# Optimization experiments

Measured on AMD Instinct MI355X. Metric: run time of the kernel, lower is better.

Reference implementation:

```python
import jax, jax.numpy as jnp
import numpy as np

N = 100000      # nodes
E = 1600000     # edges
F_IN = 256      # nfeat
F_OUT = 128     # out channels


def setup_inputs() -> dict:
    key = jax.random.key(0)
    k1, k2, k3 = jax.random.split(key, 3)
    feature = jax.random.normal(k1, (N, F_IN), dtype=jnp.float32)
    edge_index = jax.random.randint(k2, (2, E), 0, N, dtype=jnp.int32)
    # glorot-ish init for the GCN linear weight
    W = jax.random.normal(k3, (F_IN, F_OUT), dtype=jnp.float32) * (1.0 / np.sqrt(F_IN))
    b = jnp.zeros((F_OUT,), dtype=jnp.float32)
    return {"feature": feature, "edge_index": edge_index, "W": W, "b": b}


def reference(feature, edge_index, W, b):
    # GCNConv (PyG defaults): add self-loops, symmetric normalization,
    # linear transform then scatter-add aggregation to destination nodes.
    x = feature @ W                                   # [N, F_OUT]
    loops = jnp.arange(N, dtype=edge_index.dtype)
    row = jnp.concatenate([edge_index[0], loops])     # source nodes [E+N]
    col = jnp.concatenate([edge_index[1], loops])     # dest   nodes [E+N]
    ones = jnp.ones(row.shape[0], dtype=x.dtype)
    deg = jax.ops.segment_sum(ones, col, num_segments=N)   # in-degree incl. self-loop
    dinv = jnp.where(deg > 0, jax.lax.rsqrt(deg), 0.0)     # deg^{-1/2}
    norm = dinv[row] * dinv[col]                            # [E+N]
    msg = x[row] * norm[:, None]                            # gather + scale
    agg = jax.ops.segment_sum(msg, col, num_segments=N)     # scatter-add
    x_out = jax.nn.relu(agg + b)                            # [N, F_OUT]
    h = jax.nn.sigmoid(jnp.mean(x_out, axis=0))             # [F_OUT]
    return (x_out, h)
```

## Files before the change

kernel.cpp:

```cpp
#include <hip/hip_runtime.h>
#include <hip/hip_bf16.h>

typedef __attribute__((ext_vector_type(8))) short short8;
typedef __attribute__((ext_vector_type(4))) float floatx4;
typedef unsigned short u16;
typedef unsigned int u32;

#define F_IN  256
#define F_OUT 128
#define CAP   64
#define CA    24
#define CB    40
#define NWIN  8
#define PRE   24

__device__ __forceinline__ float bf_lo(u32 u) { return __uint_as_float(u << 16); }
__device__ __forceinline__ float bf_hi(u32 u) { return __uint_as_float(u & 0xffff0000u); }
__device__ __forceinline__ u16 f2bf(float f) {
    u32 u = __float_as_uint(f);
    u += 0x7fffu + ((u >> 16) & 1u);
    return (u16)(u >> 16);
}

__global__ void k_pack(const float* __restrict__ W, u16* __restrict__ Wp,
                       u16* __restrict__ xw, int* __restrict__ zero0,
                       int nzero, int N) {
    int gid = blockIdx.x * 256 + threadIdx.x;
    if (gid < 32768) {
        int f = gid >> 3, j = gid & 7;
        int lane = f & 63, tt = (f >> 6) & 7, kb = f >> 9;
        int m = lane & 15, q = lane >> 4;
        Wp[(size_t)f * 8 + j] = f2bf(W[(kb * 32 + q * 8 + j) * F_OUT + tt * 16 + m]);
    } else if (gid < 32896) {
        int e = gid - 32768;
        int w = e >> 4, m = e & 15;
        xw[((size_t)w * (N + 1) + N) * 16 + m] = 0;
    } else {
        int z = gid - 32896;
        if (z < nzero) zero0[z] = 0;
    }
}

__global__ void k_fillcap_xcd(const int* __restrict__ rowi, const int* __restrict__ coli,
                              int E, int npw, int N,
                              int* __restrict__ cursor,
                              int* __restrict__ csrA, int* __restrict__ csrB) {
    int grp  = blockIdx.x & (NWIN - 1);
    int gblk = blockIdx.x >> 3;
    int nblk = gridDim.x >> 3;
    int lo = grp * npw;
    int hi = lo + npw; if (hi > N) hi = N;
    const int stride = nblk * blockDim.x;
    int e = gblk * blockDim.x + threadIdx.x;
    for (; e + stride < E; e += 2 * stride) {
        int d0 = coli[e];
        int d1 = coli[e + stride];
        bool in0 = (d0 >= lo && d0 < hi);
        bool in1 = (d1 >= lo && d1 < hi);
        if (in0) {
            int r0 = rowi[e];
            int p = atomicAdd(&cursor[d0], 1);
            if (p < CA) csrA[d0 * CA + p] = r0;
            else if (p < CAP) csrB[d0 * CB + (p - CA)] = r0;
        }
        if (in1) {
            int r1 = rowi[e + stride];
            int p = atomicAdd(&cursor[d1], 1);
            if (p < CA) csrA[d1 * CA + p] = r1;
            else if (p < CAP) csrB[d1 * CB + (p - CA)] = r1;
        }
    }
    if (e < E) {
        int d = coli[e];
        if (d >= lo && d < hi) {
            int r = rowi[e];
            int p = atomicAdd(&cursor[d], 1);
            if (p < CA) csrA[d * CA + p] = r;
            else if (p < CAP) csrB[d * CB + (p - CA)] = r;
        }
    }
}

__global__ void k_degree(const int* __restrict__ col, int E, int* __restrict__ deg) {
    for (int e = blockIdx.x * blockDim.x + threadIdx.x; e < E; e += gridDim.x * blockDim.x)
        atomicAdd(&deg[col[e]], 1);
}

__global__ void k_blocksum(const int* __restrict__ deg, int N, int* __restrict__ bsum) {
    __shared__ int s[256];
    int base = blockIdx.x * 1024, t = threadIdx.x;
    int v = 0;
    for (int i = t; i < 1024; i += 256) { int idx = base + i; v += (idx < N) ? deg[idx] : 0; }
    s[t] = v; __syncthreads();
    for (int off = 128; off > 0; off >>= 1) {
        if (t < off) s[t] += s[t + off];
        __syncthreads();
    }
    if (t == 0) bsum[blockIdx.x] = s[0];
}

__global__ void k_rowptr(const int* __restrict__ deg, int N, const int* __restrict__ bsum,
                         int nb, int* __restrict__ rowptr) {
    __shared__ int s[256];
    __shared__ int sb[256];
    int base = blockIdx.x * 1024, t = threadIdx.x;
    sb[t] = (t < nb && t < blockIdx.x) ? bsum[t] : 0;
    __syncthreads();
    for (int off = 128; off > 0; off >>= 1) {
        if (t < off) sb[t] += sb[t + off];
        __syncthreads();
    }
    int blockbase = sb[0];
    int v[4]; int tot = 0;
#pragma unroll
    for (int j = 0; j < 4; ++j) {
        int idx = base + t * 4 + j;
        v[j] = (idx < N) ? deg[idx] : 0;
        tot += v[j];
    }
    s[t] = tot; __syncthreads();
    for (int off = 1; off < 256; off <<= 1) {
        int x = (t >= off) ? s[t - off] : 0;
        __syncthreads();
        s[t] += x;
        __syncthreads();
    }
    int prefix = blockbase + s[t] - tot;
#pragma unroll
    for (int j = 0; j < 4; ++j) {
        int idx = base + t * 4 + j;
        if (idx < N) rowptr[idx] = prefix;
        prefix += v[j];
    }
}

__global__ void k_fill(const int* __restrict__ rowi, const int* __restrict__ coli, int E,
                       const int* __restrict__ rowptr, int* __restrict__ cursor,
                       int* __restrict__ csr) {
    for (int e = blockIdx.x * blockDim.x + threadIdx.x; e < E; e += gridDim.x * blockDim.x) {
        int d = coli[e];
        int p = atomicAdd(&cursor[d], 1);
        csr[rowptr[d] + p] = rowi[e];
    }
}

__global__ __launch_bounds__(256) void k_gemm(
        const float* __restrict__ feat, const int* __restrict__ deg,
        const u16* __restrict__ Wp, u16* __restrict__ xw, int N) {
    __shared__ u16 atile[64 * 264];
    const int t = threadIdx.x, wave = t >> 6, lane = t & 63;
    const int m = lane & 15, q = lane >> 4;
    const int base = blockIdx.x * 64;

    for (int r = wave; r < 64; r += 4) {
        int i = base + r;
        float ax = 0.f, ay = 0.f, az = 0.f, aw = 0.f;
        if (i < N) {
            float di = rsqrtf((float)(deg[i] + 1));
            float4 v = *(const float4*)(feat + (size_t)i * F_IN + lane * 4);
            ax = di * v.x; ay = di * v.y; az = di * v.z; aw = di * v.w;
        }
        __hip_bfloat162 p0 = __float22bfloat162_rn(float2{ax, ay});
        __hip_bfloat162 p1 = __float22bfloat162_rn(float2{az, aw});
        u32* dst = (u32*)(atile + r * 264 + lane * 4);
        dst[0] = *(u32*)&p0;
        dst[1] = *(u32*)&p1;
    }
    __syncthreads();

    floatx4 acc[8];
#pragma unroll
    for (int tt = 0; tt < 8; ++tt) acc[tt] = (floatx4)0.0f;
    const short8* wp = (const short8*)Wp;
#pragma unroll
    for (int kb = 0; kb < 8; ++kb) {
        short8 a0 = *(const short8*)(atile + (wave * 16 + m) * 264 + kb * 32 + q * 8);
#pragma unroll
        for (int tt = 0; tt < 8; ++tt) {
            short8 b = wp[(kb * 8 + tt) * 64 + lane];
            acc[tt] = __builtin_amdgcn_mfma_f32_16x16x32_bf16(a0, b, acc[tt], 0, 0, 0);
        }
    }

#pragma unroll
    for (int r = 0; r < 4; ++r) {
        int orow = base + wave * 16 + q * 4 + r;
        if (orow < N) {
#pragma unroll
            for (int tt = 0; tt < 8; ++tt)
                xw[((size_t)tt * (N + 1) + orow) * 16 + m] = f2bf(acc[tt][r]);
        }
    }
}

__global__ __launch_bounds__(256) void k_agg(const u16* __restrict__ xw,
                                             const int* __restrict__ rowptr,
                                             const int* __restrict__ deg,
                                             const int* __restrict__ csr,
                                             const int* __restrict__ csrB,
                                             const float* __restrict__ bvec,
                                             float* __restrict__ out,
                                             float* __restrict__ hsum, int N) {
    __shared__ float hpart[16];
    int t = threadIdx.x;
    if (t < 16) hpart[t] = 0.f;
    __syncthreads();
    const int w = blockIdx.x & 7;
    const int stripe = blockIdx.x >> 3;
    const int nstripe = gridDim.x >> 3;
    const int lane = t & 63, wv = t >> 6;
    const int lane7 = lane & 7;
    const int g = lane >> 3;
    const int gbase = lane & 56;
    const u32* slice = (const u32*)xw + (size_t)w * (N + 1) * 8;
    float b0 = bvec[w * 16 + 2 * lane7], b1 = bvec[w * 16 + 2 * lane7 + 1];
    float h0 = 0.f, h1 = 0.f;
    const int step = nstripe * 32;

    int i = stripe * 32 + wv * 8 + g;
    int dd_c = 0, s0_c = 0, sA_c = N, sB_c = N, sC_c = N;
    if (i < N) {
        dd_c = deg[i];
        s0_c = rowptr ? rowptr[i] : i * CA;
        sA_c = csr[s0_c + lane7];
        sB_c = csr[s0_c + 8 + lane7];
        sC_c = csr[s0_c + 16 + lane7];
    }
    while (i < N) {
        int inext = i + step;
        int dd_n = 0, s0_n = 0, sA_n = N, sB_n = N, sC_n = N;
        if (inext < N) {
            dd_n = deg[inext];
            s0_n = rowptr ? rowptr[inext] : inext * CA;
            sA_n = csr[s0_n + lane7];
            sB_n = csr[s0_n + 8 + lane7];
            sC_n = csr[s0_n + 16 + lane7];
        }
        int dd = dd_c;
        float di = rsqrtf((float)(dd + 1));
        if (!rowptr) dd = dd < CAP ? dd : CAP;
        u32 xs = slice[(u32)(i * 8 + lane7)];
        float a0 = bf_lo(xs), a1 = bf_hi(xs);
        int sA = (lane7 < dd)      ? sA_c : N;
        int sB = (lane7 + 8 < dd)  ? sB_c : N;
        int sC = (lane7 + 16 < dd) ? sC_c : N;
        u32 xv[PRE];
#pragma unroll
        for (int u = 0; u < 8; ++u) {
            int sx = __shfl(sA, gbase + u);
            xv[u] = slice[(u32)(sx * 8 + lane7)];
        }
#pragma unroll
        for (int u = 0; u < 8; ++u) {
            int sx = __shfl(sB, gbase + u);
            xv[8 + u] = slice[(u32)(sx * 8 + lane7)];
        }
#pragma unroll
        for (int u = 0; u < 8; ++u) {
            int sx = __shfl(sC, gbase + u);
            xv[16 + u] = slice[(u32)(sx * 8 + lane7)];
        }
#pragma unroll
        for (int u = 0; u < PRE; ++u) { a0 += bf_lo(xv[u]); a1 += bf_hi(xv[u]); }
        if (__any(dd > PRE)) {
            int ddmax = dd;
            ddmax = max(ddmax, __shfl_xor(ddmax, 8));
            ddmax = max(ddmax, __shfl_xor(ddmax, 16));
            ddmax = max(ddmax, __shfl_xor(ddmax, 32));
            ddmax = min(ddmax, rowptr ? (1 << 20) : CAP);
            int s0 = s0_c;
            for (int jb = PRE; jb < ddmax; jb += 8) {
                int sxv = N;
                if (jb + lane7 < dd) {
                    if (rowptr) sxv = csr[s0 + jb + lane7];
                    else        sxv = csrB[i * CB + (jb - CA) + lane7];
                }
                u32 yv[8];
#pragma unroll
                for (int u = 0; u < 8; ++u) {
                    int sx = __shfl(sxv, gbase + u);
                    yv[u] = slice[(u32)(sx * 8 + lane7)];
                }
#pragma unroll
                for (int u = 0; u < 8; ++u) { a0 += bf_lo(yv[u]); a1 += bf_hi(yv[u]); }
            }
        }
        float o0 = fmaxf(fmaf(a0, di, b0), 0.f);
        float o1 = fmaxf(fmaf(a1, di, b1), 0.f);
        h0 += o0; h1 += o1;
        *(float2*)(out + (size_t)i * F_OUT + w * 16 + 2 * lane7) = make_float2(o0, o1);
        i = inext;
        dd_c = dd_n; s0_c = s0_n; sA_c = sA_n; sB_c = sB_n; sC_c = sC_n;
    }
    atomicAdd(&hpart[2 * lane7], h0);
    atomicAdd(&hpart[2 * lane7 + 1], h1);
    __syncthreads();
    if (t < 16) atomicAdd(&hsum[w * 16 + t], hpart[t]);
}

__global__ void k_h(const float* __restrict__ hsum, float* __restrict__ outh, float invN) {
    int t = threadIdx.x;
    if (t < 128) {
        float mm = hsum[t] * invN;
        outh[t] = 1.f / (1.f + __expf(-mm));
    }
}

extern "C" void kernel_launch(void* const* d_in, const int* in_sizes, int n_in,
                              void* d_out, int out_size, void* d_ws, size_t ws_size,
                              hipStream_t stream) {
    const float* feat = (const float*)d_in[0];
    const int* ei     = (const int*)d_in[1];
    const float* W    = (const float*)d_in[2];
    const float* bvec = (const float*)d_in[3];
    float* out        = (float*)d_out;

    const int N = in_sizes[0] / F_IN;
    const int E = in_sizes[1] / 2;

    char* ws = (char*)d_ws;
    size_t o = 0;
    u16* Wp       = (u16*)(ws + o);   o += (size_t)F_IN * F_OUT * 2;
    int* deg      = (int*)(ws + o);   o += (size_t)N * 4;
    int* cursor   = (int*)(ws + o);   o += (size_t)N * 4;
    float* hsum   = (float*)(ws + o); o += 512;
    int* rowptr   = (int*)(ws + o);   o += (size_t)N * 4;
    int* bsum     = (int*)(ws + o);   o += 1024;
    size_t fixed  = o;

    size_t xw_bytes = (size_t)(N + 1) * F_OUT * 2;
    size_t need_fast = fixed + (size_t)N * (CA + CB) * 4 + xw_bytes;
    bool fast = ws_size >= need_fast + 4096;
    int npw = (N + NWIN - 1) / NWIN;
    float invN = 1.0f / (float)N;
    float* outh = out + (size_t)N * F_OUT;

    if (fast) {
        int* csrA = (int*)(ws + o);   o += (size_t)N * CA * 4;
        int* csrB = (int*)(ws + o);   o += (size_t)N * CB * 4;
        u16* xw   = (u16*)(ws + o);   o += xw_bytes;

        int nzero = N + 128;
        int packblocks = (32896 + nzero + 255) / 256;
        k_pack<<<packblocks, 256, 0, stream>>>(W, Wp, xw, cursor, nzero, N);
        k_fillcap_xcd<<<4096, 256, 0, stream>>>(ei, ei + E, E, npw, N, cursor,
                                                csrA, csrB);
        int ntiles = (N + 63) / 64;
        k_gemm<<<ntiles, 256, 0, stream>>>(feat, cursor, Wp, xw, N);
        k_agg<<<2048, 256, 0, stream>>>(xw, nullptr, cursor, csrA, csrB,
                                        bvec, out, hsum, N);
        k_h<<<1, 128, 0, stream>>>(hsum, outh, invN);
    } else {
        int* csr = (int*)(ws + o);    o += (size_t)E * 4;
        u16* xw  = (u16*)(ws + o);    o += xw_bytes;

        hipMemsetAsync((char*)deg, 0, (size_t)N * 8 + 512, stream);
        k_pack<<<129, 256, 0, stream>>>(W, Wp, xw, cursor, 0, N);
        k_degree<<<1024, 256, 0, stream>>>(ei + E, E, deg);
        int nb = (N + 1023) / 1024;
        k_blocksum<<<nb, 256, 0, stream>>>(deg, N, bsum);
        k_rowptr<<<nb, 256, 0, stream>>>(deg, N, bsum, nb, rowptr);
        k_fill<<<1024, 256, 0, stream>>>(ei, ei + E, E, rowptr, cursor, csr);
        int ntiles = (N + 63) / 64;
        k_gemm<<<ntiles, 256, 0, stream>>>(feat, deg, Wp, xw, N);
        k_agg<<<2048, 256, 0, stream>>>(xw, rowptr, deg, csr, nullptr,
                                        bvec, out, hsum, N);
        k_h<<<1, 128, 0, stream>>>(hsum, outh, invN);
    }
}
```

Baseline: 343.4 us.

## Widen aggregation feature windows from 16 to 32 channels per slice

The bf16 projected features are now stored in 4 column-slices of 32 channels instead of 8 slices of 16, and the aggregation kernel assigns each block to one of 4 slices. Each lane gathers 8 bytes per neighbour instead of 4 and writes float4 outputs. This halves the number of index/CSR passes and shuffles per edge across slices, at the cost of a larger per-slice footprint that may fit less well in per-XCD cache and of more registers for the 64-bit prefetch buffer.

```diff
diff --git a/kernel.cpp b/kernel.cpp
--- a/kernel.cpp
+++ b/kernel.cpp
@@ -5,6 +5,7 @@
 typedef __attribute__((ext_vector_type(4))) float floatx4;
 typedef unsigned short u16;
 typedef unsigned int u32;
+typedef unsigned long long u64;
 
 #define F_IN  256
 #define F_OUT 128
@@ -12,6 +13,7 @@
 #define CA    24
 #define CB    40
 #define NWIN  8
+#define AWIN  4
 #define PRE   24
 
 __device__ __forceinline__ float bf_lo(u32 u) { return __uint_as_float(u << 16); }
@@ -33,8 +35,8 @@
         Wp[(size_t)f * 8 + j] = f2bf(W[(kb * 32 + q * 8 + j) * F_OUT + tt * 16 + m]);
     } else if (gid < 32896) {
         int e = gid - 32768;
-        int w = e >> 4, m = e & 15;
-        xw[((size_t)w * (N + 1) + N) * 16 + m] = 0;
+        int w = e >> 5, m = e & 31;
+        xw[((size_t)w * (N + 1) + N) * 32 + m] = 0;
     } else {
         int z = gid - 32896;
         if (z < nzero) zero0[z] = 0;
@@ -188,7 +190,8 @@
         if (orow < N) {
 #pragma unroll
             for (int tt = 0; tt < 8; ++tt)
-                xw[((size_t)tt * (N + 1) + orow) * 16 + m] = f2bf(acc[tt][r]);
+                xw[((size_t)(tt >> 1) * (N + 1) + orow) * 32 + (tt & 1) * 16 + m]
+                    = f2bf(acc[tt][r]);
         }
     }
 }
@@ -201,20 +204,20 @@
                                              const float* __restrict__ bvec,
                                              float* __restrict__ out,
                                              float* __restrict__ hsum, int N) {
-    __shared__ float hpart[16];
+    __shared__ float hpart[32];
     int t = threadIdx.x;
-    if (t < 16) hpart[t] = 0.f;
+    if (t < 32) hpart[t] = 0.f;
     __syncthreads();
-    const int w = blockIdx.x & 7;
-    const int stripe = blockIdx.x >> 3;
-    const int nstripe = gridDim.x >> 3;
+    const int w = blockIdx.x & (AWIN - 1);
+    const int stripe = blockIdx.x >> 2;
+    const int nstripe = gridDim.x >> 2;
     const int lane = t & 63, wv = t >> 6;
     const int lane7 = lane & 7;
     const int g = lane >> 3;
     const int gbase = lane & 56;
-    const u32* slice = (const u32*)xw + (size_t)w * (N + 1) * 8;
-    float b0 = bvec[w * 16 + 2 * lane7], b1 = bvec[w * 16 + 2 * lane7 + 1];
-    float h0 = 0.f, h1 = 0.f;
+    const u32* slice = (const u32*)xw + (size_t)w * (N + 1) * 16;
+    const float4 bv = *(const float4*)(bvec + w * 32 + lane7 * 4);
+    float h0 = 0.f, h1 = 0.f, h2 = 0.f, h3 = 0.f;
     const int step = nstripe * 32;
 
     int i = stripe * 32 + wv * 8 + g;
@@ -239,29 +242,33 @@
         int dd = dd_c;
         float di = rsqrtf((float)(dd + 1));
         if (!rowptr) dd = dd < CAP ? dd : CAP;
-        u32 xs = slice[(u32)(i * 8 + lane7)];
-        float a0 = bf_lo(xs), a1 = bf_hi(xs);
+        u64 xs = *(const u64*)(slice + (u32)(i * 16) + lane7 * 2);
+        u32 xsl = (u32)xs, xsh = (u32)(xs >> 32);
+        float a0 = bf_lo(xsl), a1 = bf_hi(xsl), a2 = bf_lo(xsh), a3 = bf_hi(xsh);
         int sA = (lane7 < dd)      ? sA_c : N;
         int sB = (lane7 + 8 < dd)  ? sB_c : N;
         int sC = (lane7 + 16 < dd) ? sC_c : N;
-        u32 xv[PRE];
+        u64 xv[PRE];
 #pragma unroll
         for (int u = 0; u < 8; ++u) {
             int sx = __shfl(sA, gbase + u);
-            xv[u] = slice[(u32)(sx * 8 + lane7)];
+            xv[u] = *(const u64*)(slice + (u32)(sx * 16) + lane7 * 2);
         }
 #pragma unroll
         for (int u = 0; u < 8; ++u) {
             int sx = __shfl(sB, gbase + u);
-            xv[8 + u] = slice[(u32)(sx * 8 + lane7)];
+            xv[8 + u] = *(const u64*)(slice + (u32)(sx * 16) + lane7 * 2);
         }
 #pragma unroll
         for (int u = 0; u < 8; ++u) {
             int sx = __shfl(sC, gbase + u);
-            xv[16 + u] = slice[(u32)(sx * 8 + lane7)];
-        }
-#pragma unroll
-        for (int u = 0; u < PRE; ++u) { a0 += bf_lo(xv[u]); a1 += bf_hi(xv[u]); }
+            xv[16 + u] = *(const u64*)(slice + (u32)(sx * 16) + lane7 * 2);
+        }
+#pragma unroll
+        for (int u = 0; u < PRE; ++u) {
+            u32 lo = (u32)xv[u], hi = (u32)(xv[u] >> 32);
+            a0 += bf_lo(lo); a1 += bf_hi(lo); a2 += bf_lo(hi); a3 += bf_hi(hi);
+        }
         if (__any(dd > PRE)) {
             int ddmax = dd;
             ddmax = max(ddmax, __shfl_xor(ddmax, 8));
@@ -275,27 +282,35 @@
                     if (rowptr) sxv = csr[s0 + jb + lane7];
                     else        sxv = csrB[i * CB + (jb - CA) + lane7];
                 }
-                u32 yv[8];
+                u64 yv[8];
 #pragma unroll
                 for (int u = 0; u < 8; ++u) {
                     int sx = __shfl(sxv, gbase + u);
-                    yv[u] = slice[(u32)(sx * 8 + lane7)];
+                    yv[u] = *(const u64*)(slice + (u32)(sx * 16) + lane7 * 2);
                 }
 #pragma unroll
-                for (int u = 0; u < 8; ++u) { a0 += bf_lo(yv[u]); a1 += bf_hi(yv[u]); }
+                for (int u = 0; u < 8; ++u) {
+                    u32 lo = (u32)yv[u], hi = (u32)(yv[u] >> 32);
+                    a0 += bf_lo(lo); a1 += bf_hi(lo); a2 += bf_lo(hi); a3 += bf_hi(hi);
+                }
             }
         }
-        float o0 = fmaxf(fmaf(a0, di, b0), 0.f);
-        float o1 = fmaxf(fmaf(a1, di, b1), 0.f);
-        h0 += o0; h1 += o1;
-        *(float2*)(out + (size_t)i * F_OUT + w * 16 + 2 * lane7) = make_float2(o0, o1);
+        float o0 = fmaxf(fmaf(a0, di, bv.x), 0.f);
+        float o1 = fmaxf(fmaf(a1, di, bv.y), 0.f);
+        float o2 = fmaxf(fmaf(a2, di, bv.z), 0.f);
+        float o3 = fmaxf(fmaf(a3, di, bv.w), 0.f);
+        h0 += o0; h1 += o1; h2 += o2; h3 += o3;
+        *(float4*)(out + (size_t)i * F_OUT + w * 32 + lane7 * 4) =
+            make_float4(o0, o1, o2, o3);
         i = inext;
         dd_c = dd_n; s0_c = s0_n; sA_c = sA_n; sB_c = sB_n; sC_c = sC_n;
     }
-    atomicAdd(&hpart[2 * lane7], h0);
-    atomicAdd(&hpart[2 * lane7 + 1], h1);
+    atomicAdd(&hpart[lane7 * 4 + 0], h0);
+    atomicAdd(&hpart[lane7 * 4 + 1], h1);
+    atomicAdd(&hpart[lane7 * 4 + 2], h2);
+    atomicAdd(&hpart[lane7 * 4 + 3], h3);
     __syncthreads();
-    if (t < 16) atomicAdd(&hsum[w * 16 + t], hpart[t]);
+    if (t < 32) atomicAdd(&hsum[w * 32 + t], hpart[t]);
 }
 
 __global__ void k_h(const float* __restrict__ hsum, float* __restrict__ outh, float invN) {
```

Result: faster. 328.8 us (-4.2%).
